# Optimization experiments

Hardware: AMD Instinct MI355X
Metric: run time of the kernel (lower is better)

## Reference

```python
import jax, jax.numpy as jnp
import numpy as np


def setup_inputs() -> dict:
    key = jax.random.key(0)
    kx, ky = jax.random.split(key)
    n, m, d = 2048, 2048, 16  # d == n_wires
    x = jax.random.normal(kx, (n, d), dtype=jnp.float32)
    y = jax.random.normal(ky, (m, d), dtype=jnp.float32)
    return {"x": x, "y": y}


def reference(x, y):
    # RY gates on distinct wires commute; RY(-y_k) RY(x_k) = RY(x_k - y_k).
    # State = tensor product over wires of RY(x_k - y_k)|0>, so the |0...0>
    # amplitude is prod_k cos((x_k - y_k)/2). Original code stores abs(amplitude).
    half_diff = 0.5 * (x[:, None, :] - y[None, :, :])  # [n, m, d]
    kernel = jnp.abs(jnp.prod(jnp.cos(half_diff), axis=-1))  # [n, m]
    return kernel
```

## Files before the change

### kernel.cpp

```cpp
#include <hip/hip_runtime.h>
#include <hip/hip_bf16.h>


constexpr int D = 16;
constexpr int RSTR = 72;

typedef short  bf16x8 __attribute__((ext_vector_type(8)));
typedef float  f32x16 __attribute__((ext_vector_type(16)));

static __device__ inline unsigned int pk2(float a, float b) {
    __hip_bfloat16 ha = __float2bfloat16(a);
    __hip_bfloat16 hb = __float2bfloat16(b);
    unsigned short ua, ub;
    __builtin_memcpy(&ua, &ha, 2);
    __builtin_memcpy(&ub, &hb, 2);
    return (unsigned int)ua | ((unsigned int)ub << 16);
}

__global__ __launch_bounds__(256)
void qkern(const float* __restrict__ x, const float* __restrict__ y,
           float* __restrict__ out, int m) {
    __shared__ unsigned short Al[128 * RSTR];
    __shared__ unsigned short Bl[128 * RSTR];

    const int tid   = threadIdx.x;
    const int row0b = blockIdx.x * 128;
    const int col0b = blockIdx.y * 128;

    {
        const int u = tid;
        const bool isrow = (u < 128);
        const float* src = isrow ? (x + (size_t)(row0b + u) * D)
                                 : (y + (size_t)(col0b + (u - 128)) * D);
        unsigned short* dst = isrow ? (Al + (size_t)u * RSTR)
                                    : (Bl + (size_t)(u - 128) * RSTR);
        const float scale = isrow ? 0.5f : 1.0f;

        float f[8][4];
#pragma unroll
        for (int p = 0; p < 8; ++p) {
            const float a0 = src[2 * p], a1 = src[2 * p + 1];
            float sm, cm, sp, cp;
            __sincosf(0.5f * (a0 - a1), &sm, &cm);
            __sincosf(0.5f * (a0 + a1), &sp, &cp);
            f[p][0] = scale * cm; f[p][1] = scale * sm;
            f[p][2] = scale * cp; f[p][3] = scale * sp;
        }
#pragma unroll
        for (int q = 0; q < 4; ++q) {
            const float* fa = f[2 * q];
            const float* fb = f[2 * q + 1];
            uint4 lo, hi;
            lo.x = pk2(fa[0] * fb[0], fa[0] * fb[1]);
            lo.y = pk2(fa[0] * fb[2], fa[0] * fb[3]);
            lo.z = pk2(fa[1] * fb[0], fa[1] * fb[1]);
            lo.w = pk2(fa[1] * fb[2], fa[1] * fb[3]);
            hi.x = pk2(fa[2] * fb[0], fa[2] * fb[1]);
            hi.y = pk2(fa[2] * fb[2], fa[2] * fb[3]);
            hi.z = pk2(fa[3] * fb[0], fa[3] * fb[1]);
            hi.w = pk2(fa[3] * fb[2], fa[3] * fb[3]);
            *(uint4*)(dst + q * 16)     = lo;
            *(uint4*)(dst + q * 16 + 8) = hi;
        }
    }
    __syncthreads();

    const int wave = tid >> 6;
    const int lane = tid & 63;
    const int l31  = lane & 31;
    const int kh   = lane >> 5;
    const int rw   = wave * 32;

    const f32x16 zc = {0.f};

    bf16x8 af[4];
#pragma unroll
    for (int q = 0; q < 4; ++q)
        af[q] = *(const bf16x8*)(Al + (size_t)(rw + l31) * RSTR + q * 16 + kh * 8);

#pragma unroll
    for (int cb = 0; cb < 4; ++cb) {
        const int cw = cb * 32;
        f32x16 prod;
        {
            const bf16x8 b0 = *(const bf16x8*)(Bl + (size_t)(cw + l31) * RSTR + kh * 8);
            prod = __builtin_amdgcn_mfma_f32_32x32x16_bf16(af[0], b0, zc, 0, 0, 0);
        }
#pragma unroll
        for (int q = 1; q < 4; ++q) {
            const bf16x8 bq = *(const bf16x8*)(Bl + (size_t)(cw + l31) * RSTR + q * 16 + kh * 8);
            const f32x16 acc = __builtin_amdgcn_mfma_f32_32x32x16_bf16(af[q], bq, zc, 0, 0, 0);
            prod *= acc;
        }

        float* base = out + (size_t)(row0b + rw + 4 * kh) * m + col0b + cw + l31;
#pragma unroll
        for (int r = 0; r < 16; ++r) {
            const int row_off = (r & 3) + 8 * (r >> 2);
            __builtin_nontemporal_store(fabsf(prod[r]), base + (size_t)row_off * m);
        }
    }
}

extern "C" void kernel_launch(void* const* d_in, const int* in_sizes, int n_in,
                              void* d_out, int out_size, void* d_ws, size_t ws_size,
                              hipStream_t stream) {
    const float* x = (const float*)d_in[0];
    const float* y = (const float*)d_in[1];
    float* out = (float*)d_out;
    const int n = in_sizes[0] / D;
    const int m = in_sizes[1] / D;

    dim3 grid(n / 128, m / 128);
    qkern<<<grid, 256, 0, stream>>>(x, y, out, m);
}
```

Measured before the change: 61.16 us.

## Halve column tile to 64 and split Y-row feature prep across thread pairs

The column tile shrinks from 128 to 64, which doubles the grid to 512 blocks and halves the per-block MFMA and store work. This gives more blocks to spread across CUs and shortens each block's tail. Y-side feature construction now uses two threads per row, each handling half the wire pairs, so all 256 threads stay busy during the prologue. The bf16 pack now uses a paired float2 conversion. In exchange, the x-side sincos prologue is recomputed twice as often across the grid.

After: 61.43 us. About the same (+0.5%).

```diff
diff --git a/kernel.cpp b/kernel.cpp
--- a/kernel.cpp
+++ b/kernel.cpp
@@ -9,33 +9,40 @@
 typedef float  f32x16 __attribute__((ext_vector_type(16)));
 
 static __device__ inline unsigned int pk2(float a, float b) {
-    __hip_bfloat16 ha = __float2bfloat16(a);
-    __hip_bfloat16 hb = __float2bfloat16(b);
-    unsigned short ua, ub;
-    __builtin_memcpy(&ua, &ha, 2);
-    __builtin_memcpy(&ub, &hb, 2);
-    return (unsigned int)ua | ((unsigned int)ub << 16);
+    __hip_bfloat162 h = __float22bfloat162_rn(make_float2(a, b));
+    unsigned int u;
+    __builtin_memcpy(&u, &h, 4);
+    return u;
+}
+
+static __device__ inline void emit_quad(unsigned short* dst, int q,
+                                        const float* fa, const float* fb) {
+    uint4 lo, hi;
+    lo.x = pk2(fa[0] * fb[0], fa[0] * fb[1]);
+    lo.y = pk2(fa[0] * fb[2], fa[0] * fb[3]);
+    lo.z = pk2(fa[1] * fb[0], fa[1] * fb[1]);
+    lo.w = pk2(fa[1] * fb[2], fa[1] * fb[3]);
+    hi.x = pk2(fa[2] * fb[0], fa[2] * fb[1]);
+    hi.y = pk2(fa[2] * fb[2], fa[2] * fb[3]);
+    hi.z = pk2(fa[3] * fb[0], fa[3] * fb[1]);
+    hi.w = pk2(fa[3] * fb[2], fa[3] * fb[3]);
+    *(uint4*)(dst + q * 16)     = lo;
+    *(uint4*)(dst + q * 16 + 8) = hi;
 }
 
 __global__ __launch_bounds__(256)
 void qkern(const float* __restrict__ x, const float* __restrict__ y,
            float* __restrict__ out, int m) {
     __shared__ unsigned short Al[128 * RSTR];
-    __shared__ unsigned short Bl[128 * RSTR];
+    __shared__ unsigned short Bl[64 * RSTR];
 
     const int tid   = threadIdx.x;
     const int row0b = blockIdx.x * 128;
-    const int col0b = blockIdx.y * 128;
+    const int col0b = blockIdx.y * 64;
 
-    {
-        const int u = tid;
-        const bool isrow = (u < 128);
-        const float* src = isrow ? (x + (size_t)(row0b + u) * D)
-                                 : (y + (size_t)(col0b + (u - 128)) * D);
-        unsigned short* dst = isrow ? (Al + (size_t)u * RSTR)
-                                    : (Bl + (size_t)(u - 128) * RSTR);
-        const float scale = isrow ? 0.5f : 1.0f;
-
+    if (tid < 128) {
+        const float* src = x + (size_t)(row0b + tid) * D;
+        unsigned short* dst = Al + (size_t)tid * RSTR;
         float f[8][4];
 #pragma unroll
         for (int p = 0; p < 8; ++p) {
@@ -43,25 +50,31 @@
             float sm, cm, sp, cp;
             __sincosf(0.5f * (a0 - a1), &sm, &cm);
             __sincosf(0.5f * (a0 + a1), &sp, &cp);
-            f[p][0] = scale * cm; f[p][1] = scale * sm;
-            f[p][2] = scale * cp; f[p][3] = scale * sp;
+            f[p][0] = 0.5f * cm; f[p][1] = 0.5f * sm;
+            f[p][2] = 0.5f * cp; f[p][3] = 0.5f * sp;
         }
 #pragma unroll
-        for (int q = 0; q < 4; ++q) {
-            const float* fa = f[2 * q];
-            const float* fb = f[2 * q + 1];
-            uint4 lo, hi;
-            lo.x = pk2(fa[0] * fb[0], fa[0] * fb[1]);
-            lo.y = pk2(fa[0] * fb[2], fa[0] * fb[3]);
-            lo.z = pk2(fa[1] * fb[0], fa[1] * fb[1]);
-            lo.w = pk2(fa[1] * fb[2], fa[1] * fb[3]);
-            hi.x = pk2(fa[2] * fb[0], fa[2] * fb[1]);
-            hi.y = pk2(fa[2] * fb[2], fa[2] * fb[3]);
-            hi.z = pk2(fa[3] * fb[0], fa[3] * fb[1]);
-            hi.w = pk2(fa[3] * fb[2], fa[3] * fb[3]);
-            *(uint4*)(dst + q * 16)     = lo;
-            *(uint4*)(dst + q * 16 + 8) = hi;
+        for (int q = 0; q < 4; ++q)
+            emit_quad(dst, q, f[2 * q], f[2 * q + 1]);
+    } else {
+        const int u    = (tid - 128) >> 1;
+        const int half = tid & 1;
+        const float* src = y + (size_t)(col0b + u) * D;
+        unsigned short* dst = Bl + (size_t)u * RSTR;
+        float f[4][4];
+#pragma unroll
+        for (int pp = 0; pp < 4; ++pp) {
+            const int p = half * 4 + pp;
+            const float a0 = src[2 * p], a1 = src[2 * p + 1];
+            float sm, cm, sp, cp;
+            __sincosf(0.5f * (a0 - a1), &sm, &cm);
+            __sincosf(0.5f * (a0 + a1), &sp, &cp);
+            f[pp][0] = cm; f[pp][1] = sm;
+            f[pp][2] = cp; f[pp][3] = sp;
         }
+#pragma unroll
+        for (int qq = 0; qq < 2; ++qq)
+            emit_quad(dst, half * 2 + qq, f[2 * qq], f[2 * qq + 1]);
     }
     __syncthreads();
 
@@ -79,7 +92,7 @@
         af[q] = *(const bf16x8*)(Al + (size_t)(rw + l31) * RSTR + q * 16 + kh * 8);
 
 #pragma unroll
-    for (int cb = 0; cb < 4; ++cb) {
+    for (int cb = 0; cb < 2; ++cb) {
         const int cw = cb * 32;
         f32x16 prod;
         {
@@ -111,6 +124,6 @@
     const int n = in_sizes[0] / D;
     const int m = in_sizes[1] / D;
 
-    dim3 grid(n / 128, m / 128);
+    dim3 grid(n / 128, m / 64);
     qkern<<<grid, 256, 0, stream>>>(x, y, out, m);
 }
```
